# Kernel tuning notes

Measured on AMD Instinct MI355X. Metric: run time of the kernel, lower is better.

Reference implementation:

```python
import jax, jax.numpy as jnp
import numpy as np

HIDDEN = 4096
INTER = 14336
POOL = 16384   # total tokens in the routing pool
NSEL = 4096    # tokens routed to this expert


def setup_inputs() -> dict:
    key = jax.random.key(0)
    ks = jax.random.split(key, 6)
    x = jax.random.normal(ks[0], (POOL, HIDDEN), dtype=jnp.float32)
    top_x = jax.random.randint(ks[1], (NSEL,), 0, POOL, dtype=jnp.int64)
    weight = jax.random.uniform(ks[2], (NSEL,), dtype=jnp.float32)
    s = 1.0 / np.sqrt(HIDDEN)
    Wg = jax.random.uniform(ks[3], (INTER, HIDDEN), dtype=jnp.float32, minval=-s, maxval=s)
    Wu = jax.random.uniform(ks[4], (INTER, HIDDEN), dtype=jnp.float32, minval=-s, maxval=s)
    s2 = 1.0 / np.sqrt(INTER)
    Wd = jax.random.uniform(ks[5], (HIDDEN, INTER), dtype=jnp.float32, minval=-s2, maxval=s2)
    return {"x": x, "Wg": Wg, "Wu": Wu, "Wd": Wd, "top_x": top_x, "weight": weight}


def reference(x, Wg, Wu, Wd, top_x, weight):
    # gather selected tokens: [n, H]
    x_sel = jnp.take(x, top_x, axis=0)
    # gate / up projections: [n, I]
    g = jnp.einsum('nh,ih->ni', x_sel, Wg)
    u = jnp.einsum('nh,ih->ni', x_sel, Wu)
    # SwiGLU activation (drop is identity at eval)
    h = jax.nn.silu(g) * u
    # weighted down projection: per-token routing weight applied to output
    out = jnp.einsum('ni,hi->nh', h, Wd) * weight[:, None]
    # slice [0:batch_size] where batch_size = top_x.shape[0] (identity here)
    return out[: top_x.shape[0], :]
```

## Files before the change

### kernel.cpp

```cpp
#include <hip/hip_runtime.h>
#include <hip/hip_bf16.h>
#include <stdint.h>

#define HIDDEN 4096
#define INTER  14336
#define NSEL   4096

using short8 = __attribute__((ext_vector_type(8))) short;
using f32x4  = __attribute__((ext_vector_type(4))) float;

__device__ __forceinline__ uint16_t f2bf(float f) {
  uint32_t u = __float_as_uint(f);
  uint32_t r = (u + 0x7FFFu + ((u >> 16) & 1u)) >> 16;
  return (uint16_t)r;
}
__device__ __forceinline__ uint32_t pack2(float lo, float hi) {
  return (uint32_t)f2bf(lo) | ((uint32_t)f2bf(hi) << 16);
}

__global__ void prep(const float* __restrict__ x, const int* __restrict__ idx,
                     uint16_t* __restrict__ xs,
                     const float* __restrict__ Wg, uint16_t* __restrict__ w1,
                     const float* __restrict__ Wu, uint16_t* __restrict__ w2,
                     const float* __restrict__ Wd, uint16_t* __restrict__ w3,
                     int ncvt) {
  const int b = blockIdx.x;
  const int t = threadIdx.x;
  if (b < NSEL) {
    const size_t s = (size_t)idx[b] * HIDDEN + (size_t)t * 16;
    const size_t d = (size_t)b * HIDDEN + (size_t)t * 16;
    const float4* sp = (const float4*)(x + s);
    float4 f0 = sp[0], f1 = sp[1], f2 = sp[2], f3 = sp[3];
    uint4 v0, v1;
    v0.x = pack2(f0.x, f0.y); v0.y = pack2(f0.z, f0.w);
    v0.z = pack2(f1.x, f1.y); v0.w = pack2(f1.z, f1.w);
    v1.x = pack2(f2.x, f2.y); v1.y = pack2(f2.z, f2.w);
    v1.z = pack2(f3.x, f3.y); v1.w = pack2(f3.z, f3.w);
    *(uint4*)(xs + d)     = v0;
    *(uint4*)(xs + d + 8) = v1;
    return;
  }
  int cb = b - NSEL;
  const float* src; uint16_t* dst;
  if (cb < ncvt)            { src = Wg; dst = w1; }
  else if (cb < 2 * ncvt)   { src = Wu; dst = w2; cb -= ncvt; }
  else                      { src = Wd; dst = w3; cb -= 2 * ncvt; }
#pragma unroll
  for (int k = 0; k < 8; ++k) {
    const size_t i = (size_t)cb * 16384 + (size_t)k * 2048 + (size_t)t * 8;
    float4 a = *(const float4*)(src + i);
    float4 c = *(const float4*)(src + i + 4);
    uint4 v;
    v.x = pack2(a.x, a.y); v.y = pack2(a.z, a.w);
    v.z = pack2(c.x, c.y); v.w = pack2(c.z, c.w);
    *(uint4*)(dst + i) = v;
  }
}

__device__ __forceinline__ void gload16(const void* g, void* l) {
  __builtin_amdgcn_global_load_lds(
      (const __attribute__((address_space(1))) void*)g,
      (__attribute__((address_space(3))) void*)l, 16, 0, 0);
}

__device__ __forceinline__ float silu(float g) {
  return g / (1.f + __expf(-g));
}

template<int MODE>
__global__ __launch_bounds__(1024, 4) void gemm_f(
    const uint16_t* __restrict__ A,
    const uint16_t* __restrict__ B0,
    const uint16_t* __restrict__ B1,
    uint16_t* __restrict__ G,
    float* __restrict__ O,
    const float* __restrict__ Wt,
    int N, int K)
{
  __shared__ __align__(16) uint16_t lds[3][16384];

  const int nwg = (int)gridDim.x;
  const int bid = (int)blockIdx.x;
  const int lid = (bid & 7) * (nwg >> 3) + (bid >> 3);
  const int bm = lid & 15, bn = lid >> 4;

  const int tid  = (int)threadIdx.x;
  const int lane = tid & 63, w = tid >> 6;
  const int lr = lane & 15, lg = lane >> 4;

  int wm, wn, s;
  if constexpr (MODE == 0) { s = w >> 3; wm = w & 3; wn = (w >> 2) & 1; }
  else                     { s = 0;      wm = w & 3; wn = w >> 2;       }

  int offA[4], offB[4];
#pragma unroll
  for (int m = 0; m < 4; ++m) {
    const int r = wm * 64 + m * 16 + lr;
    offA[m] = (r >> 1) * 64 + (((((r & 1) << 2) | lg) ^ ((r >> 1) & 7)) * 8);
  }
  const int bBase = (MODE == 0) ? (8192 + s * 4096) : 8192;
#pragma unroll
  for (int n = 0; n < 4; ++n) {
    const int r = wn * 64 + n * 16 + lr;
    offB[n] = bBase + (r >> 1) * 64 + (((((r & 1) << 2) | lg) ^ ((r >> 1) & 7)) * 8);
  }

  const int suA   = (tid & 7) ^ ((tid >> 3) & 7);
  const int sRowA = 2 * (tid >> 3) + (suA >> 2);
  const int sColA = (suA & 3) * 8;
  const uint16_t* aSrc = A + (size_t)(bm * 256 + sRowA) * K + sColA;
  const int jB    = (MODE == 0) ? (tid & 511) : tid;
  const int suB   = (jB & 7) ^ ((jB >> 3) & 7);
  const int sRowB = 2 * (jB >> 3) + (suB >> 2);
  const int sColB = (suB & 3) * 8;
  const uint16_t* bSel = (MODE == 0) ? ((tid < 512) ? B0 : B1) : B0;
  const uint16_t* bSrc = bSel + (size_t)(bn * ((MODE == 0) ? 128 : 256) + sRowB) * K + sColB;
  const int bDst = (MODE == 0) ? (8192 + (tid >> 9) * 4096 + (tid & 511) * 8)
                               : (8192 + tid * 8);

#define STAGE(tt, sl) do { \
    gload16(aSrc + (size_t)(tt) * 32, &lds[sl][tid * 8]); \
    gload16(bSrc + (size_t)(tt) * 32, &lds[sl][bDst]); \
  } while (0)

  f32x4 acc[4][4];
#pragma unroll
  for (int m = 0; m < 4; ++m)
#pragma unroll
    for (int n = 0; n < 4; ++n)
#pragma unroll
      for (int j = 0; j < 4; ++j) acc[m][n][j] = 0.f;

  const int nk = K >> 5;

  STAGE(0, 0);
  STAGE(1, 1);
  asm volatile("s_waitcnt vmcnt(2)" ::: "memory");
  __builtin_amdgcn_s_barrier();

  for (int t = 0; t < nk; ++t) {
    const uint16_t* S = &lds[t % 3][0];

    if (t + 2 < nk) STAGE(t + 2, (t + 2) % 3);

    short8 av[4], bv[4];
#pragma unroll
    for (int m = 0; m < 4; ++m) av[m] = *(const short8*)&S[offA[m]];
#pragma unroll
    for (int n = 0; n < 4; ++n) bv[n] = *(const short8*)&S[offB[n]];

    __builtin_amdgcn_s_setprio(1);
#pragma unroll
    for (int m = 0; m < 4; ++m)
#pragma unroll
      for (int n = 0; n < 4; ++n)
        acc[m][n] = __builtin_amdgcn_mfma_f32_16x16x32_bf16(av[m], bv[n], acc[m][n], 0, 0, 0);
    __builtin_amdgcn_s_setprio(0);

    if (t + 2 < nk) { asm volatile("s_waitcnt vmcnt(2)" ::: "memory"); }
    else            { asm volatile("s_waitcnt vmcnt(0)" ::: "memory"); }
    __builtin_amdgcn_s_barrier();
  }
#undef STAGE

  if constexpr (MODE == 1) {
    const int row0 = bm * 256 + wm * 64, col0 = bn * 256 + wn * 64;
#pragma unroll
    for (int m = 0; m < 4; ++m)
#pragma unroll
      for (int n = 0; n < 4; ++n) {
        const int c  = col0 + n * 16 + lr;
        const int rb = row0 + m * 16 + lg * 4;
#pragma unroll
        for (int j = 0; j < 4; ++j) {
          const int r = rb + j;
          __builtin_nontemporal_store(acc[m][n][j] * Wt[r], &O[(size_t)r * N + c]);
        }
      }
  } else {
    float* X = (float*)&lds[0][0];
    const int row0 = bm * 256 + wm * 64, col0 = bn * 128 + wn * 64;
#pragma unroll
    for (int m = 0; m < 4; ++m) {
      __builtin_amdgcn_s_barrier();
      if (s == 0) {
#pragma unroll
        for (int n = 0; n < 4; ++n)
          *(f32x4*)&X[w * 1024 + n * 256 + lr * 16 + lg * 4] = acc[m][n];
      }
      __builtin_amdgcn_s_barrier();
      if (s == 1) {
#pragma unroll
        for (int n = 0; n < 4; ++n) {
          const f32x4 g4 = *(const f32x4*)&X[(w - 8) * 1024 + n * 256 + lr * 16 + lg * 4];
          const int c  = col0 + n * 16 + lr;
          const int rb = row0 + m * 16 + lg * 4;
#pragma unroll
          for (int j = 0; j < 4; ++j)
            G[(size_t)(rb + j) * N + c] = f2bf(silu(g4[j]) * acc[m][n][j]);
        }
      }
    }
  }
}

extern "C" void kernel_launch(void* const* d_in, const int* in_sizes, int n_in,
                              void* d_out, int out_size, void* d_ws, size_t ws_size,
                              hipStream_t stream) {
  const float* x   = (const float*)d_in[0];
  const float* Wg  = (const float*)d_in[1];
  const float* Wu  = (const float*)d_in[2];
  const float* Wd  = (const float*)d_in[3];
  const int*   top = (const int*)d_in[4];
  const float* wt  = (const float*)d_in[5];
  float* out = (float*)d_out;

  const size_t NE_X = (size_t)NSEL * HIDDEN;
  const size_t NE_W = (size_t)INTER * HIDDEN;
  if (ws_size < (NE_X + 3 * NE_W + NE_W) * sizeof(uint16_t)) return;

  uint16_t* xs = (uint16_t*)d_ws;
  uint16_t* w1 = xs + NE_X;
  uint16_t* w2 = w1 + NE_W;
  uint16_t* w3 = w2 + NE_W;
  uint16_t* gh = w3 + NE_W;

  const int NCVT = (int)(NE_W / 16384);
  const int ngGU = 16 * (INTER / 128);
  const int ngDN = 16 * (HIDDEN / 256);

  prep<<<NSEL + 3 * NCVT, 256, 0, stream>>>(x, top, xs, Wg, w1, Wu, w2, Wd, w3, NCVT);

  gemm_f<0><<<ngGU, 1024, 0, stream>>>(xs, w1, w2, gh, nullptr, nullptr,
                                       INTER, HIDDEN);
  gemm_f<1><<<ngDN, 1024, 0, stream>>>(gh, w3, nullptr, nullptr, out, wt,
                                       HIDDEN, INTER);
}
```

Baseline: 1.418 ms.

## Load GEMM A operand directly from global memory and swizzle epilogue LDS

Each wave now reads its A fragments straight from global memory into registers instead of staging them through LDS. Only the B tile stays in the triple-buffered LDS pipeline, which halves the LDS footprint. The epilogue scratch layout is XOR-swizzled to reduce bank conflicts on the gate handoff. The cost is that A loads are not prefetched: they are issued at the top of each iteration and waited on before the MFMAs. Each A row is also fetched redundantly by several waves, so global-load latency and cache traffic can become exposed.

```diff
diff --git a/kernel.cpp b/kernel.cpp
--- a/kernel.cpp
+++ b/kernel.cpp
@@ -77,7 +77,7 @@
     const float* __restrict__ Wt,
     int N, int K)
 {
-  __shared__ __align__(16) uint16_t lds[3][16384];
+  __shared__ __align__(16) uint16_t lds[3][8192];
 
   const int nwg = (int)gridDim.x;
   const int bid = (int)blockIdx.x;
@@ -92,36 +92,27 @@
   if constexpr (MODE == 0) { s = w >> 3; wm = w & 3; wn = (w >> 2) & 1; }
   else                     { s = 0;      wm = w & 3; wn = w >> 2;       }
 
-  int offA[4], offB[4];
-#pragma unroll
-  for (int m = 0; m < 4; ++m) {
-    const int r = wm * 64 + m * 16 + lr;
-    offA[m] = (r >> 1) * 64 + (((((r & 1) << 2) | lg) ^ ((r >> 1) & 7)) * 8);
-  }
-  const int bBase = (MODE == 0) ? (8192 + s * 4096) : 8192;
+  const uint16_t* aBase = A + (size_t)(bm * 256 + wm * 64 + lr) * K + lg * 8;
+  const size_t aMstep = (size_t)16 * K;
+
+  int offB[4];
+  const int bBase = (MODE == 0) ? s * 4096 : 0;
 #pragma unroll
   for (int n = 0; n < 4; ++n) {
     const int r = wn * 64 + n * 16 + lr;
     offB[n] = bBase + (r >> 1) * 64 + (((((r & 1) << 2) | lg) ^ ((r >> 1) & 7)) * 8);
   }
 
-  const int suA   = (tid & 7) ^ ((tid >> 3) & 7);
-  const int sRowA = 2 * (tid >> 3) + (suA >> 2);
-  const int sColA = (suA & 3) * 8;
-  const uint16_t* aSrc = A + (size_t)(bm * 256 + sRowA) * K + sColA;
   const int jB    = (MODE == 0) ? (tid & 511) : tid;
   const int suB   = (jB & 7) ^ ((jB >> 3) & 7);
   const int sRowB = 2 * (jB >> 3) + (suB >> 2);
   const int sColB = (suB & 3) * 8;
   const uint16_t* bSel = (MODE == 0) ? ((tid < 512) ? B0 : B1) : B0;
   const uint16_t* bSrc = bSel + (size_t)(bn * ((MODE == 0) ? 128 : 256) + sRowB) * K + sColB;
-  const int bDst = (MODE == 0) ? (8192 + (tid >> 9) * 4096 + (tid & 511) * 8)
-                               : (8192 + tid * 8);
-
-#define STAGE(tt, sl) do { \
-    gload16(aSrc + (size_t)(tt) * 32, &lds[sl][tid * 8]); \
-    gload16(bSrc + (size_t)(tt) * 32, &lds[sl][bDst]); \
-  } while (0)
+  const int bDst = (MODE == 0) ? ((tid >> 9) * 4096 + (tid & 511) * 8)
+                               : (tid * 8);
+
+#define STAGE_B(tt, sl) gload16(bSrc + (size_t)(tt) * 32, &lds[sl][bDst])
 
   f32x4 acc[4][4];
 #pragma unroll
@@ -133,19 +124,25 @@
 
   const int nk = K >> 5;
 
-  STAGE(0, 0);
-  STAGE(1, 1);
-  asm volatile("s_waitcnt vmcnt(2)" ::: "memory");
+  STAGE_B(0, 0);
+  STAGE_B(1, 1);
+  asm volatile("s_waitcnt vmcnt(1)" ::: "memory");
   __builtin_amdgcn_s_barrier();
 
   for (int t = 0; t < nk; ++t) {
     const uint16_t* S = &lds[t % 3][0];
 
-    if (t + 2 < nk) STAGE(t + 2, (t + 2) % 3);
-
-    short8 av[4], bv[4];
-#pragma unroll
-    for (int m = 0; m < 4; ++m) av[m] = *(const short8*)&S[offA[m]];
+    short8 av[4];
+#pragma unroll
+    for (int m = 0; m < 4; ++m)
+      av[m] = *(const short8*)(aBase + (size_t)m * aMstep + (size_t)t * 32);
+
+    if (t + 2 < nk) STAGE_B(t + 2, (t + 2) % 3);
+
+    if (t + 2 < nk) { asm volatile("s_waitcnt vmcnt(1)" ::: "memory"); }
+    else            { asm volatile("s_waitcnt vmcnt(0)" ::: "memory"); }
+
+    short8 bv[4];
 #pragma unroll
     for (int n = 0; n < 4; ++n) bv[n] = *(const short8*)&S[offB[n]];
 
@@ -157,11 +154,9 @@
         acc[m][n] = __builtin_amdgcn_mfma_f32_16x16x32_bf16(av[m], bv[n], acc[m][n], 0, 0, 0);
     __builtin_amdgcn_s_setprio(0);
 
-    if (t + 2 < nk) { asm volatile("s_waitcnt vmcnt(2)" ::: "memory"); }
-    else            { asm volatile("s_waitcnt vmcnt(0)" ::: "memory"); }
     __builtin_amdgcn_s_barrier();
   }
-#undef STAGE
+#undef STAGE_B
 
   if constexpr (MODE == 1) {
     const int row0 = bm * 256 + wm * 64, col0 = bn * 256 + wn * 64;
@@ -179,6 +174,7 @@
       }
   } else {
     float* X = (float*)&lds[0][0];
+    const int xo = lr * 16 + ((lg ^ ((lr >> 1) & 3)) * 4);
     const int row0 = bm * 256 + wm * 64, col0 = bn * 128 + wn * 64;
 #pragma unroll
     for (int m = 0; m < 4; ++m) {
@@ -186,13 +182,13 @@
       if (s == 0) {
 #pragma unroll
         for (int n = 0; n < 4; ++n)
-          *(f32x4*)&X[w * 1024 + n * 256 + lr * 16 + lg * 4] = acc[m][n];
+          *(f32x4*)&X[w * 1024 + n * 256 + xo] = acc[m][n];
       }
       __builtin_amdgcn_s_barrier();
       if (s == 1) {
 #pragma unroll
         for (int n = 0; n < 4; ++n) {
-          const f32x4 g4 = *(const f32x4*)&X[(w - 8) * 1024 + n * 256 + lr * 16 + lg * 4];
+          const f32x4 g4 = *(const f32x4*)&X[(w - 8) * 1024 + n * 256 + xo];
           const int c  = col0 + n * 16 + lr;
           const int rb = row0 + m * 16 + lg * 4;
 #pragma unroll
@@ -217,7 +213,7 @@
 
   const size_t NE_X = (size_t)NSEL * HIDDEN;
   const size_t NE_W = (size_t)INTER * HIDDEN;
-  if (ws_size < (NE_X + 3 * NE_W + NE_W) * sizeof(uint16_t)) return;
+  if (ws_size < (NE_X + 4 * NE_W) * sizeof(uint16_t)) return;
 
   uint16_t* xs = (uint16_t*)d_ws;
   uint16_t* w1 = xs + NE_X;
```

Measured after the change: 3.585 ms. 2.53x slower.

## Overlap Wd conversion with gate/up GEMM, deepen LDS pipeline, swizzle epilogue

Applied to the files above, without the earlier changes.

Moves the fp32-to-bf16 conversion of Wd out of the prep kernel and into extra workgroups appended to the gate/up GEMM launch, so that conversion can overlap with GEMM work instead of sitting on the serial path. The GEMM's LDS pipeline goes from 3 stages to 4, with three tiles prefetched ahead, to hide more global-load latency. The cost is 128KB of LDS per workgroup. The epilogue's LDS staging layout is XOR-swizzled to reduce bank conflicts. Because the conversion blocks sit at the highest block IDs, they may be scheduled last and fail to overlap, and the larger LDS footprint can lower occupancy.

```diff
diff --git a/kernel.cpp b/kernel.cpp
--- a/kernel.cpp
+++ b/kernel.cpp
@@ -22,7 +22,6 @@
                      uint16_t* __restrict__ xs,
                      const float* __restrict__ Wg, uint16_t* __restrict__ w1,
                      const float* __restrict__ Wu, uint16_t* __restrict__ w2,
-                     const float* __restrict__ Wd, uint16_t* __restrict__ w3,
                      int ncvt) {
   const int b = blockIdx.x;
   const int t = threadIdx.x;
@@ -42,9 +41,8 @@
   }
   int cb = b - NSEL;
   const float* src; uint16_t* dst;
-  if (cb < ncvt)            { src = Wg; dst = w1; }
-  else if (cb < 2 * ncvt)   { src = Wu; dst = w2; cb -= ncvt; }
-  else                      { src = Wd; dst = w3; cb -= 2 * ncvt; }
+  if (cb < ncvt) { src = Wg; dst = w1; }
+  else           { src = Wu; dst = w2; cb -= ncvt; }
 #pragma unroll
   for (int k = 0; k < 8; ++k) {
     const size_t i = (size_t)cb * 16384 + (size_t)k * 2048 + (size_t)t * 8;
@@ -75,16 +73,32 @@
     uint16_t* __restrict__ G,
     float* __restrict__ O,
     const float* __restrict__ Wt,
-    int N, int K)
+    int N, int K, int nGemm,
+    const float* __restrict__ cvtIn, uint16_t* __restrict__ cvtOut)
 {
-  __shared__ __align__(16) uint16_t lds[3][16384];
-
-  const int nwg = (int)gridDim.x;
+  __shared__ __align__(16) uint16_t lds[4][16384];
+
   const int bid = (int)blockIdx.x;
-  const int lid = (bid & 7) * (nwg >> 3) + (bid >> 3);
+  const int tid = (int)threadIdx.x;
+
+  if (MODE == 0 && bid >= nGemm) {
+    const int cb = bid - nGemm;
+#pragma unroll
+    for (int k = 0; k < 8; ++k) {
+      const size_t i = (size_t)cb * 65536 + (size_t)k * 8192 + (size_t)tid * 8;
+      float4 a = *(const float4*)(cvtIn + i);
+      float4 c = *(const float4*)(cvtIn + i + 4);
+      uint4 v;
+      v.x = pack2(a.x, a.y); v.y = pack2(a.z, a.w);
+      v.z = pack2(c.x, c.y); v.w = pack2(c.z, c.w);
+      *(uint4*)(cvtOut + i) = v;
+    }
+    return;
+  }
+
+  const int lid = (bid & 7) * (nGemm >> 3) + (bid >> 3);
   const int bm = lid & 15, bn = lid >> 4;
 
-  const int tid  = (int)threadIdx.x;
   const int lane = tid & 63, w = tid >> 6;
   const int lr = lane & 15, lg = lane >> 4;
 
@@ -109,6 +123,7 @@
   const int sRowA = 2 * (tid >> 3) + (suA >> 2);
   const int sColA = (suA & 3) * 8;
   const uint16_t* aSrc = A + (size_t)(bm * 256 + sRowA) * K + sColA;
+
   const int jB    = (MODE == 0) ? (tid & 511) : tid;
   const int suB   = (jB & 7) ^ ((jB >> 3) & 7);
   const int sRowB = 2 * (jB >> 3) + (suB >> 2);
@@ -135,13 +150,14 @@
 
   STAGE(0, 0);
   STAGE(1, 1);
-  asm volatile("s_waitcnt vmcnt(2)" ::: "memory");
+  STAGE(2, 2);
+  asm volatile("s_waitcnt vmcnt(4)" ::: "memory");
   __builtin_amdgcn_s_barrier();
 
   for (int t = 0; t < nk; ++t) {
-    const uint16_t* S = &lds[t % 3][0];
-
-    if (t + 2 < nk) STAGE(t + 2, (t + 2) % 3);
+    const uint16_t* S = &lds[t & 3][0];
+
+    if (t + 3 < nk) STAGE(t + 3, (t + 3) & 3);
 
     short8 av[4], bv[4];
 #pragma unroll
@@ -157,8 +173,9 @@
         acc[m][n] = __builtin_amdgcn_mfma_f32_16x16x32_bf16(av[m], bv[n], acc[m][n], 0, 0, 0);
     __builtin_amdgcn_s_setprio(0);
 
-    if (t + 2 < nk) { asm volatile("s_waitcnt vmcnt(2)" ::: "memory"); }
-    else            { asm volatile("s_waitcnt vmcnt(0)" ::: "memory"); }
+    if      (t + 3 < nk) { asm volatile("s_waitcnt vmcnt(4)" ::: "memory"); }
+    else if (t + 2 < nk) { asm volatile("s_waitcnt vmcnt(2)" ::: "memory"); }
+    else                 { asm volatile("s_waitcnt vmcnt(0)" ::: "memory"); }
     __builtin_amdgcn_s_barrier();
   }
 #undef STAGE
@@ -179,6 +196,7 @@
       }
   } else {
     float* X = (float*)&lds[0][0];
+    const int xo = lr * 16 + ((lg ^ ((lr >> 1) & 3)) * 4);
     const int row0 = bm * 256 + wm * 64, col0 = bn * 128 + wn * 64;
 #pragma unroll
     for (int m = 0; m < 4; ++m) {
@@ -186,13 +204,13 @@
       if (s == 0) {
 #pragma unroll
         for (int n = 0; n < 4; ++n)
-          *(f32x4*)&X[w * 1024 + n * 256 + lr * 16 + lg * 4] = acc[m][n];
+          *(f32x4*)&X[w * 1024 + n * 256 + xo] = acc[m][n];
       }
       __builtin_amdgcn_s_barrier();
       if (s == 1) {
 #pragma unroll
         for (int n = 0; n < 4; ++n) {
-          const f32x4 g4 = *(const f32x4*)&X[(w - 8) * 1024 + n * 256 + lr * 16 + lg * 4];
+          const f32x4 g4 = *(const f32x4*)&X[(w - 8) * 1024 + n * 256 + xo];
           const int c  = col0 + n * 16 + lr;
           const int rb = row0 + m * 16 + lg * 4;
 #pragma unroll
@@ -217,7 +235,7 @@
 
   const size_t NE_X = (size_t)NSEL * HIDDEN;
   const size_t NE_W = (size_t)INTER * HIDDEN;
-  if (ws_size < (NE_X + 3 * NE_W + NE_W) * sizeof(uint16_t)) return;
+  if (ws_size < (NE_X + 4 * NE_W) * sizeof(uint16_t)) return;
 
   uint16_t* xs = (uint16_t*)d_ws;
   uint16_t* w1 = xs + NE_X;
@@ -226,13 +244,14 @@
   uint16_t* gh = w3 + NE_W;
 
   const int NCVT = (int)(NE_W / 16384);
+  const int NCVT_GU = (int)(NE_W / 65536);
   const int ngGU = 16 * (INTER / 128);
   const int ngDN = 16 * (HIDDEN / 256);
 
-  prep<<<NSEL + 3 * NCVT, 256, 0, stream>>>(x, top, xs, Wg, w1, Wu, w2, Wd, w3, NCVT);
-
-  gemm_f<0><<<ngGU, 1024, 0, stream>>>(xs, w1, w2, gh, nullptr, nullptr,
-                                       INTER, HIDDEN);
+  prep<<<NSEL + 2 * NCVT, 256, 0, stream>>>(x, top, xs, Wg, w1, Wu, w2, NCVT);
+
+  gemm_f<0><<<ngGU + NCVT_GU, 1024, 0, stream>>>(xs, w1, w2, gh, nullptr, nullptr,
+                                                 INTER, HIDDEN, ngGU, Wd, w3);
   gemm_f<1><<<ngDN, 1024, 0, stream>>>(gh, w3, nullptr, nullptr, out, wt,
-                                       HIDDEN, INTER);
-}
+                                       HIDDEN, INTER, ngDN, nullptr, nullptr);
+}
```

Result: no change. 1.396 ms (-1.5%).
